# Kernel tuning notes

Hardware: AMD Instinct MI355X
Metric: run time of the kernel (lower is better)

## Reference

```python
import jax, jax.numpy as jnp
import numpy as np

B, L, D, H = 2, 2048, 2048, 16
Dh = D // H
THETA = 10000.0
NEG = -1e9


def _rope_tables(length, offset=0):
    # inv_freq: [Dh/2], positions: [L]
    inv_freq = 1.0 / (THETA ** (jnp.arange(0, Dh, 2, dtype=jnp.float32) / Dh))
    pos = jnp.arange(offset, offset + length, dtype=jnp.float32)
    freqs = pos[:, None] * inv_freq[None, :]           # [L, Dh/2]
    emb = jnp.concatenate([freqs, freqs], axis=-1)     # [L, Dh]
    return jnp.cos(emb), jnp.sin(emb)


def _rotate_half(t):
    t1, t2 = t[..., : Dh // 2], t[..., Dh // 2:]
    return jnp.concatenate([-t2, t1], axis=-1)


def setup_inputs() -> dict:
    key = jax.random.key(0)
    k1, k2, k3 = jax.random.split(key, 3)
    x = jax.random.normal(k1, (B, L, D), dtype=jnp.float32)
    attention_mask = jnp.ones((B, L), dtype=jnp.int32)
    w_qkv = jax.random.normal(k2, (D, 3 * D), dtype=jnp.float32) * (D ** -0.5)
    w_proj = jax.random.normal(k3, (D, D), dtype=jnp.float32) * (D ** -0.5)
    return {"x": x, "attention_mask": attention_mask, "w_qkv": w_qkv, "w_proj": w_proj}


def reference(x, attention_mask, w_qkv, w_proj):
    # QKV projection (no bias)
    qkv = x @ w_qkv                                    # [B, L, 3D]
    q, k, v = jnp.split(qkv, 3, axis=-1)
    q = q.reshape(B, L, H, Dh).transpose(0, 2, 1, 3)   # [B, H, L, Dh]
    k = k.reshape(B, L, H, Dh).transpose(0, 2, 1, 3)
    v = v.reshape(B, L, H, Dh).transpose(0, 2, 1, 3)

    # RoPE (past_len = 0)
    cos, sin = _rope_tables(L)                         # [L, Dh]
    q = q * cos + _rotate_half(q) * sin
    k = k * cos + _rotate_half(k) * sin

    # causal + key-padding mask (True = masked out)
    causal = jnp.triu(jnp.ones((L, L), dtype=bool), k=1)         # [L, L]
    pad = (attention_mask == 0)[:, None, None, :]                # [B,1,1,L]
    mask = causal[None, None, :, :] | pad                        # [B,1,L,L]

    scale = Dh ** -0.5
    scores = jnp.einsum("bhqd,bhkd->bhqk", q, k) * scale         # [B,H,L,L]
    scores = jnp.where(mask, NEG, scores)
    attn = jax.nn.softmax(scores, axis=-1)
    y = jnp.einsum("bhqk,bhkd->bhqd", attn, v)                   # [B,H,L,Dh]
    y = y.transpose(0, 2, 1, 3).reshape(B, L, D)
    return y @ w_proj
```

## Files before the change

kernel.cpp:

```cpp
#include <hip/hip_runtime.h>
#include <hip/hip_bf16.h>

typedef unsigned short ushort_t;
typedef __attribute__((ext_vector_type(4))) float fvec4;
typedef __attribute__((ext_vector_type(16))) float fvec16;
typedef __attribute__((ext_vector_type(8))) short short8;
typedef __attribute__((ext_vector_type(4))) unsigned short usvec4;
typedef __attribute__((ext_vector_type(2))) unsigned int uvec2;

typedef const __attribute__((address_space(1))) void* gas_ptr;
typedef __attribute__((address_space(3))) void* las_ptr;

__device__ __forceinline__ void glds16(const void* g, void* l) {
  __builtin_amdgcn_global_load_lds((gas_ptr)g, (las_ptr)l, 16, 0, 0);
}

__device__ __forceinline__ ushort_t f2bf(float f) {
  unsigned u = __float_as_uint(f);
  u += 0x7FFFu + ((u >> 16) & 1u);
  return (ushort_t)(u >> 16);
}
__device__ __forceinline__ float bf2f(ushort_t h) {
  return __uint_as_float(((unsigned)h) << 16);
}

__device__ __forceinline__ void swap32(unsigned& a, unsigned& b) {
#if __has_builtin(__builtin_amdgcn_permlane32_swap)
  uvec2 r = __builtin_amdgcn_permlane32_swap(a, b, false, false);
  a = r[0]; b = r[1];
#else
  const unsigned sa = (unsigned)__shfl_xor((int)a, 32);
  const unsigned sb = (unsigned)__shfl_xor((int)b, 32);
  const bool hi = (threadIdx.x & 32) != 0;
  const unsigned na = hi ? sb : a;
  const unsigned nb = hi ? b : sa;
  a = na; b = nb;
#endif
}

__global__ __launch_bounds__(256) void cast_f32_bf16(const float* __restrict__ X,
                                                     ushort_t* __restrict__ Xb) {
  const size_t i = ((size_t)blockIdx.x * 256 + threadIdx.x) * 4;
  const fvec4 v = *(const fvec4*)(X + i);
  usvec4 o;
  o[0] = f2bf(v[0]); o[1] = f2bf(v[1]); o[2] = f2bf(v[2]); o[3] = f2bf(v[3]);
  *(usvec4*)(Xb + i) = o;
}

__global__ __launch_bounds__(256) void tcast(const float* __restrict__ W,
                                             ushort_t* __restrict__ Wt,
                                             const int Kd, const int Nd) {
  __shared__ float ls[64][65];
  const int t = threadIdx.x;
  const int n0 = blockIdx.x * 64, k0 = blockIdx.y * 64;
  const int kr = t >> 4, nc = (t & 15) * 4;
#pragma unroll
  for (int it = 0; it < 4; ++it) {
    const fvec4 v = *(const fvec4*)(W + (size_t)(k0 + it * 16 + kr) * Nd + n0 + nc);
    ls[it * 16 + kr][nc + 0] = v[0];
    ls[it * 16 + kr][nc + 1] = v[1];
    ls[it * 16 + kr][nc + 2] = v[2];
    ls[it * 16 + kr][nc + 3] = v[3];
  }
  __syncthreads();
  const int nr = t >> 2, kg = (t & 3) * 16;
  __align__(16) ushort_t tmp[16];
#pragma unroll
  for (int i = 0; i < 16; ++i) tmp[i] = f2bf(ls[kg + i][nr]);
  ushort_t* dst = Wt + (size_t)(n0 + nr) * Kd + k0 + kg;
  *(short8*)(dst)     = *(const short8*)(tmp);
  *(short8*)(dst + 8) = *(const short8*)(tmp + 8);
}

#define FENCE asm volatile("" ::: "memory")

__device__ __forceinline__ void stage_unit(const ushort_t* __restrict__ G, const int rbase,
                                           const int K, const int tk,
                                           ushort_t* ldsmat, const int u,
                                           const int wv, const int lane) {
  const int rr = lane >> 3;
  const int kk = ((lane & 7) ^ rr) * 8;
  const int r64 = wv * 8 + rr;
  glds16(G + (size_t)(rbase + u * 64 + r64) * K + tk + kk,
         ldsmat + (((u * 2 + 0) * 64 + wv * 8) * 64));
  glds16(G + (size_t)(rbase + 128 + u * 64 + r64) * K + tk + kk,
         ldsmat + (((u * 2 + 1) * 64 + wv * 8) * 64));
}

__device__ __forceinline__ short8 frag_ld(const ushort_t* ldsmat, const int rbase,
                                          const int kc, const int quad, const int mm) {
  const int r = rbase + mm;
  const int blk = r >> 6;
  const int pblk = ((blk & 1) << 1) | (blk >> 1);
  const int ldsrow = pblk * 64 + (r & 63);
  const int kb = (kc * 64 + quad * 16) ^ ((mm & 7) << 4);
  return *(const short8*)(ldsmat + ldsrow * 64 + (kb >> 1));
}

#define LD_A4(s_, q_)                                                         \
  short8 af[2][2];                                                            \
  af[0][0] = frag_ld(&lds[s_][0][0], wr * 128 + (q_) * 32,      0, quad, mm); \
  af[0][1] = frag_ld(&lds[s_][0][0], wr * 128 + (q_) * 32,      1, quad, mm); \
  af[1][0] = frag_ld(&lds[s_][0][0], wr * 128 + (q_) * 32 + 16, 0, quad, mm); \
  af[1][1] = frag_ld(&lds[s_][0][0], wr * 128 + (q_) * 32 + 16, 1, quad, mm);

#define LD_B8(s_)                                                             \
  _Pragma("unroll")                                                           \
  for (int j = 0; j < 4; ++j) {                                               \
    bfr[j][0] = frag_ld(&lds[s_][1][0], wc * 64 + j * 16, 0, quad, mm);       \
    bfr[j][1] = frag_ld(&lds[s_][1][0], wc * 64 + j * 16, 1, quad, mm);       \
  }

#define MFMA16(q_)                                                            \
  __builtin_amdgcn_s_setprio(1);                                              \
  _Pragma("unroll")                                                           \
  for (int ii = 0; ii < 2; ++ii)                                              \
  _Pragma("unroll")                                                           \
  for (int j = 0; j < 4; ++j) {                                               \
    acc[(q_) * 2 + ii][j] = __builtin_amdgcn_mfma_f32_16x16x32_bf16(          \
        af[ii][0], bfr[j][0], acc[(q_) * 2 + ii][j], 0, 0, 0);                \
    acc[(q_) * 2 + ii][j] = __builtin_amdgcn_mfma_f32_16x16x32_bf16(          \
        af[ii][1], bfr[j][1], acc[(q_) * 2 + ii][j], 0, 0, 0);                \
  }                                                                           \
  __builtin_amdgcn_s_setprio(0);

__global__ __launch_bounds__(512, 2) void gemm256(
    const ushort_t* __restrict__ A, const ushort_t* __restrict__ Bt,
    const int M, const int N, const int K, const int mode,
    float* __restrict__ C,
    ushort_t* __restrict__ Qo, ushort_t* __restrict__ Ko, ushort_t* __restrict__ Vo) {
  __shared__ __align__(16) ushort_t lds[2][2][16384];

  const int tid = threadIdx.x, wv = tid >> 6, lane = tid & 63;
  const int quad = lane >> 4, mm = lane & 15;
  const int wr = wv >> 2, wc = wv & 3;

  const int nwg = gridDim.x, ntx = N >> 8;
  const int bid = blockIdx.x;
  const int swz = (bid & 7) * (nwg >> 3) + (bid >> 3);
  const int by = swz / ntx, bx = swz - by * ntx;
  const int row0 = by * 256, col0 = bx * 256;

  fvec4 acc[8][4];
#pragma unroll
  for (int i = 0; i < 8; ++i)
#pragma unroll
    for (int j = 0; j < 4; ++j) acc[i][j] = (fvec4){0.f, 0.f, 0.f, 0.f};

  short8 bfr[4][2];

  stage_unit(Bt, col0, K, 0,  &lds[0][1][0], 0, wv, lane); FENCE;
  stage_unit(Bt, col0, K, 0,  &lds[0][1][0], 1, wv, lane); FENCE;
  stage_unit(A,  row0, K, 0,  &lds[0][0][0], 0, wv, lane); FENCE;
  stage_unit(A,  row0, K, 0,  &lds[0][0][0], 1, wv, lane); FENCE;
  stage_unit(Bt, col0, K, 64, &lds[1][1][0], 0, wv, lane); FENCE;
  stage_unit(Bt, col0, K, 64, &lds[1][1][0], 1, wv, lane); FENCE;
  stage_unit(A,  row0, K, 64, &lds[1][0][0], 0, wv, lane); FENCE;
  asm volatile("s_waitcnt vmcnt(6)" ::: "memory");
  __builtin_amdgcn_s_barrier();

  const int nit = K >> 7;
  for (int i = 0; i < nit; ++i) {
    const bool more = (i + 1 < nit);
    const int kA = i * 128 + 64;
    const int kB = i * 128 + 128;
    const int kC = i * 128 + 192;
    { __builtin_amdgcn_s_barrier();
      LD_A4(0, 0); LD_B8(0);
      stage_unit(A, row0, K, kA, &lds[1][0][0], 1, wv, lane);
      MFMA16(0); }
    { __builtin_amdgcn_s_barrier();
      LD_A4(0, 1);
      if (more) stage_unit(Bt, col0, K, kB, &lds[0][1][0], 0, wv, lane);
      MFMA16(1); }
    { __builtin_amdgcn_s_barrier();
      LD_A4(0, 2);
      if (more) stage_unit(Bt, col0, K, kB, &lds[0][1][0], 1, wv, lane);
      MFMA16(2); }
    { __builtin_amdgcn_s_barrier();
      LD_A4(0, 3);
      if (more) { stage_unit(A, row0, K, kB, &lds[0][0][0], 0, wv, lane);
        asm volatile("s_waitcnt vmcnt(6)" ::: "memory");
      } else { asm volatile("s_waitcnt vmcnt(0)" ::: "memory"); }
      MFMA16(3); }
    { __builtin_amdgcn_s_barrier();
      LD_A4(1, 0); LD_B8(1);
      if (more) stage_unit(A, row0, K, kB, &lds[0][0][0], 1, wv, lane);
      MFMA16(0); }
    { __builtin_amdgcn_s_barrier();
      LD_A4(1, 1);
      if (more) stage_unit(Bt, col0, K, kC, &lds[1][1][0], 0, wv, lane);
      MFMA16(1); }
    { __builtin_amdgcn_s_barrier();
      LD_A4(1, 2);
      if (more) stage_unit(Bt, col0, K, kC, &lds[1][1][0], 1, wv, lane);
      MFMA16(2); }
    { __builtin_amdgcn_s_barrier();
      LD_A4(1, 3);
      if (more) { stage_unit(A, row0, K, kC, &lds[1][0][0], 0, wv, lane);
        asm volatile("s_waitcnt vmcnt(6)" ::: "memory"); }
      MFMA16(3); }
  }

  if (mode == 0) {
#pragma unroll
    for (int i = 0; i < 8; ++i)
#pragma unroll
      for (int r = 0; r < 4; ++r) {
        const int row = row0 + wr * 128 + i * 16 + quad * 4 + r;
        float* cr = C + (size_t)row * N + col0 + wc * 64;
#pragma unroll
        for (int j = 0; j < 4; ++j) cr[j * 16 + mm] = acc[i][j][r];
      }
  } else {
    const int gcol = col0 + wc * 64;
    const int which = gcol >> 11;
    const int h = (gcol >> 7) & 15;
    const int coff = gcol & 127;
    ushort_t* dst = (which == 0) ? Qo : (which == 1) ? Ko : Vo;
#pragma unroll
    for (int i = 0; i < 8; ++i)
#pragma unroll
      for (int r = 0; r < 4; ++r) {
        const int row = row0 + wr * 128 + i * 16 + quad * 4 + r;
        const int bb = row >> 11, l = row & 2047;
        ushort_t* dr = dst + ((size_t)(bb * 16 + h) * 2048 + l) * 128 + coff;
#pragma unroll
        for (int j = 0; j < 4; ++j) dr[j * 16 + mm] = f2bf(acc[i][j][r]);
      }
  }
}

__device__ __forceinline__ void stage_a128(const ushort_t* __restrict__ G, const int row0,
                                           const int K, const int tk, ushort_t* ldsA,
                                           const int wv, const int lane) {
  const int rr = lane >> 3;
  const int kk = ((lane & 7) ^ rr) * 8;
  const int r = wv * 8 + rr;
  glds16(G + (size_t)(row0 + r) * K + tk + kk,      ldsA + (wv * 8) * 64);
  glds16(G + (size_t)(row0 + 64 + r) * K + tk + kk, ldsA + (64 + wv * 8) * 64);
}
__device__ __forceinline__ void stage_b128(const ushort_t* __restrict__ G, const int col0,
                                           const int K, const int tk, ushort_t* ldsB,
                                           const int u, const int wv, const int lane) {
  const int rr = lane >> 3;
  const int kk = ((lane & 7) ^ rr) * 8;
  const int r = u * 64 + wv * 8 + rr;
  glds16(G + (size_t)(col0 + r) * K + tk + kk,       ldsB + (u * 64 + wv * 8) * 64);
  glds16(G + (size_t)(col0 + 128 + r) * K + tk + kk, ldsB + (128 + u * 64 + wv * 8) * 64);
}
__device__ __forceinline__ short8 fragld128(const ushort_t* mat, const int row,
                                            const int kc, const int quad) {
  const int kb = (kc * 64 + quad * 16) ^ ((row & 7) << 4);
  return *(const short8*)(mat + row * 64 + (kb >> 1));
}

__global__ __launch_bounds__(512, 2) void gemm128(
    const ushort_t* __restrict__ A, const ushort_t* __restrict__ Bt,
    const int M, const int N, const int K, const int mode,
    float* __restrict__ C,
    ushort_t* __restrict__ Qo, ushort_t* __restrict__ Ko, ushort_t* __restrict__ Vo) {
  __shared__ __align__(16) ushort_t l128[2][24576];

  const int tid = threadIdx.x, wv = tid >> 6, lane = tid & 63;
  const int quad = lane >> 4, mm = lane & 15;
  const int wr = wv >> 2, wc = wv & 3;

  const int nwg = gridDim.x, ntx = N >> 8;
  const int bid = blockIdx.x;
  const int swz = (bid & 7) * (nwg >> 3) + (bid >> 3);
  const int by = swz / ntx, bx = swz - by * ntx;
  const int row0 = by * 128, col0 = bx * 256;

  fvec4 acc[4][4];
#pragma unroll
  for (int m = 0; m < 4; ++m)
#pragma unroll
    for (int j = 0; j < 4; ++j) acc[m][j] = (fvec4){0.f, 0.f, 0.f, 0.f};

  ushort_t* A0 = &l128[0][0];     ushort_t* B0 = &l128[0][8192];
  ushort_t* A1 = &l128[1][0];     ushort_t* B1 = &l128[1][8192];

  short8 bfr[4][2];

  stage_b128(Bt, col0, K, 0,  B0, 0, wv, lane); FENCE;
  stage_b128(Bt, col0, K, 0,  B0, 1, wv, lane); FENCE;
  stage_a128(A,  row0, K, 0,  A0,    wv, lane); FENCE;
  stage_b128(Bt, col0, K, 64, B1, 0, wv, lane); FENCE;
  stage_b128(Bt, col0, K, 64, B1, 1, wv, lane); FENCE;
  asm volatile("s_waitcnt vmcnt(4)" ::: "memory");
  __builtin_amdgcn_s_barrier();

  const int nit = K >> 7;
  for (int i = 0; i < nit; ++i) {
    const bool more = (i + 1 < nit);
    const int kA = i * 128 + 64;
    const int kB = i * 128 + 128;
    const int kC = i * 128 + 192;
    {
      stage_a128(A, row0, K, kA, A1, wv, lane);
      short8 af[4];
#pragma unroll
      for (int m = 0; m < 4; ++m) af[m] = fragld128(A0, wr * 64 + m * 16 + mm, 0, quad);
#pragma unroll
      for (int j = 0; j < 4; ++j) {
        bfr[j][0] = fragld128(B0, wc * 64 + j * 16 + mm, 0, quad);
        bfr[j][1] = fragld128(B0, wc * 64 + j * 16 + mm, 1, quad);
      }
      __builtin_amdgcn_s_setprio(1);
#pragma unroll
      for (int m = 0; m < 4; ++m)
#pragma unroll
        for (int j = 0; j < 4; ++j)
          acc[m][j] = __builtin_amdgcn_mfma_f32_16x16x32_bf16(af[m], bfr[j][0], acc[m][j], 0, 0, 0);
      __builtin_amdgcn_s_setprio(0);
      asm volatile("s_waitcnt lgkmcnt(0)" ::: "memory");
      __builtin_amdgcn_sched_barrier(0);
    }
    {
      __builtin_amdgcn_s_barrier();
      if (more) { stage_b128(Bt, col0, K, kB, B0, 0, wv, lane); FENCE;
                  stage_b128(Bt, col0, K, kB, B0, 1, wv, lane); FENCE; }
      if (more) { asm volatile("s_waitcnt vmcnt(4)" ::: "memory"); }
      else      { asm volatile("s_waitcnt vmcnt(0)" ::: "memory"); }
      short8 af[4];
#pragma unroll
      for (int m = 0; m < 4; ++m) af[m] = fragld128(A0, wr * 64 + m * 16 + mm, 1, quad);
      __builtin_amdgcn_s_setprio(1);
#pragma unroll
      for (int m = 0; m < 4; ++m)
#pragma unroll
        for (int j = 0; j < 4; ++j)
          acc[m][j] = __builtin_amdgcn_mfma_f32_16x16x32_bf16(af[m], bfr[j][1], acc[m][j], 0, 0, 0);
      __builtin_amdgcn_s_setprio(0);
    }
    {
      __builtin_amdgcn_s_barrier();
      if (more) stage_a128(A, row0, K, kB, A0, wv, lane);
      short8 af[4];
#pragma unroll
      for (int m = 0; m < 4; ++m) af[m] = fragld128(A1, wr * 64 + m * 16 + mm, 0, quad);
#pragma unroll
      for (int j = 0; j < 4; ++j) {
        bfr[j][0] = fragld128(B1, wc * 64 + j * 16 + mm, 0, quad);
        bfr[j][1] = fragld128(B1, wc * 64 + j * 16 + mm, 1, quad);
      }
      __builtin_amdgcn_s_setprio(1);
#pragma unroll
      for (int m = 0; m < 4; ++m)
#pragma unroll
        for (int j = 0; j < 4; ++j)
          acc[m][j] = __builtin_amdgcn_mfma_f32_16x16x32_bf16(af[m], bfr[j][0], acc[m][j], 0, 0, 0);
      __builtin_amdgcn_s_setprio(0);
      asm volatile("s_waitcnt lgkmcnt(0)" ::: "memory");
      __builtin_amdgcn_sched_barrier(0);
    }
    {
      __builtin_amdgcn_s_barrier();
      if (more) { stage_b128(Bt, col0, K, kC, B1, 0, wv, lane); FENCE;
                  stage_b128(Bt, col0, K, kC, B1, 1, wv, lane); FENCE;
                  asm volatile("s_waitcnt vmcnt(4)" ::: "memory"); }
      short8 af[4];
#pragma unroll
      for (int m = 0; m < 4; ++m) af[m] = fragld128(A1, wr * 64 + m * 16 + mm, 1, quad);
      __builtin_amdgcn_s_setprio(1);
#pragma unroll
      for (int m = 0; m < 4; ++m)
#pragma unroll
        for (int j = 0; j < 4; ++j)
          acc[m][j] = __builtin_amdgcn_mfma_f32_16x16x32_bf16(af[m], bfr[j][1], acc[m][j], 0, 0, 0);
      __builtin_amdgcn_s_setprio(0);
      __builtin_amdgcn_s_barrier();
    }
  }

  if (mode == 0) {
#pragma unroll
    for (int m = 0; m < 4; ++m)
#pragma unroll
      for (int r = 0; r < 4; ++r) {
        const int row = row0 + wr * 64 + m * 16 + quad * 4 + r;
        float* cr = C + (size_t)row * N + col0 + wc * 64;
#pragma unroll
        for (int j = 0; j < 4; ++j) cr[j * 16 + mm] = acc[m][j][r];
      }
  } else {
    const int gcol = col0 + wc * 64;
    const int which = gcol >> 11;
    const int h = (gcol >> 7) & 15;
    const int coff = gcol & 127;
    ushort_t* dst = (which == 0) ? Qo : (which == 1) ? Ko : Vo;
#pragma unroll
    for (int m = 0; m < 4; ++m)
#pragma unroll
      for (int r = 0; r < 4; ++r) {
        const int row = row0 + wr * 64 + m * 16 + quad * 4 + r;
        const int bb = row >> 11, l = row & 2047;
        ushort_t* dr = dst + ((size_t)(bb * 16 + h) * 2048 + l) * 128 + coff;
#pragma unroll
        for (int j = 0; j < 4; ++j) dr[j * 16 + mm] = f2bf(acc[m][j][r]);
      }
  }
}

__global__ __launch_bounds__(256) void rope_kernel(ushort_t* Qb, ushort_t* Kb) {
  const int gid = blockIdx.x * 256 + threadIdx.x;
  const int pd = gid & 63;
  const int row = gid >> 6;
  const int l = row & 2047;
  ushort_t* base = (blockIdx.y ? Kb : Qb) + (size_t)row * 128;
  const float a = bf2f(base[pd]);
  const float bv = bf2f(base[pd + 64]);
  const float invf_rev = exp2f(-(float)pd * 0.20762050593045702f) * 0.15915494309189535f;
  float rev = (float)l * invf_rev;
  rev -= floorf(rev);
  const float ang = rev * 6.283185307179586f;
  float s, c;
  __sincosf(ang, &s, &c);
  float na = a * c - bv * s;
  float nb = bv * c + a * s;
  if (blockIdx.y == 0) { na *= 0.08838834764831845f; nb *= 0.08838834764831845f; }
  base[pd] = f2bf(na);
  base[pd + 64] = f2bf(nb);
}

__global__ __launch_bounds__(256) void vtrans_kernel(const ushort_t* __restrict__ Vn,
                                                     ushort_t* __restrict__ Vt) {
  __shared__ ushort_t ls[128 * 132];
  const int bh = blockIdx.x >> 4;
  const int l0 = (blockIdx.x & 15) * 128;
  const int t = threadIdx.x;
  const ushort_t* src = Vn + ((size_t)bh * 2048 + l0) * 128;
#pragma unroll
  for (int it = 0; it < 16; ++it) {
    const int c = it * 256 + t;
    const int lr = c >> 5, dc = (c & 31) * 4;
    *(usvec4*)(ls + lr * 132 + dc) = *(const usvec4*)(src + lr * 128 + dc);
  }
  __syncthreads();
  ushort_t* dstb = Vt + (size_t)bh * 128 * 2048 + l0;
#pragma unroll
  for (int it = 0; it < 16; ++it) {
    const int c = it * 256 + t;
    const int d = c >> 5, lc = (c & 31) * 4;
    usvec4 o;
    o[0] = ls[(lc + 0) * 132 + d];
    o[1] = ls[(lc + 1) * 132 + d];
    o[2] = ls[(lc + 2) * 132 + d];
    o[3] = ls[(lc + 3) * 132 + d];
    *(usvec4*)(dstb + (size_t)d * 2048 + lc) = o;
  }
}

__global__ __launch_bounds__(256, 2) void flash_kernel(
    const ushort_t* __restrict__ Qb, const ushort_t* __restrict__ Kb,
    const ushort_t* __restrict__ Vt, const int* __restrict__ am,
    ushort_t* __restrict__ Y) {
  __shared__ __align__(16) ushort_t lK[2][8192];
  __shared__ __align__(16) ushort_t lV[2][8192];
  __shared__ float lds_l[128];

  const int tid = threadIdx.x, wv = tid >> 6, lane = tid & 63;
  const int lh = lane >> 5, cq = lane & 31;
  const int bid = blockIdx.x;
  const int bh = bid & 31;
  const int qi = 15 - (bid >> 5);
  const int b = bh >> 4, head = bh & 15;
  const size_t qkBase = (size_t)bh * (2048 * 128);
  const int qb = qi * 128 + wv * 32;
  const int q = qb + cq;

  unsigned fullbits = 0;
  {
    const int* amr = am + b * 2048;
#pragma unroll
    for (int rgn = 0; rgn < 4; ++rgn) {
      const int4 a0 = *(const int4*)(amr + rgn * 512 + lane * 8);
      const int4 a1 = *(const int4*)(amr + rgn * 512 + lane * 8 + 4);
      const bool ok8 = a0.x && a0.y && a0.z && a0.w && a1.x && a1.y && a1.z && a1.w;
      const unsigned long long bal = __ballot(ok8);
#pragma unroll
      for (int tt = 0; tt < 8; ++tt)
        fullbits |= ((((bal >> (8 * tt)) & 0xFFull) == 0xFFull) ? 1u : 0u) << (rgn * 8 + tt);
    }
  }

  short8 qf[8];
  {
    const ushort_t* qrow = Qb + qkBase + (size_t)q * 128;
#pragma unroll
    for (int c = 0; c < 8; ++c) qf[c] = *(const short8*)(qrow + c * 16 + lh * 8);
  }

  fvec16 yacc[4];
#pragma unroll
  for (int i = 0; i < 4; ++i)
#pragma unroll
    for (int r = 0; r < 16; ++r) yacc[i][r] = 0.f;
  float psum = 0.f;

#define FLASH_STAGE(dK, dV, kk0)                                                          \
  _Pragma("unroll")                                                                       \
  for (int it = 0; it < 4; ++it) {                                                        \
    const int f_ = it * 4 + wv;                                                           \
    const int ct_ = f_ >> 3, c_ = f_ & 7;                                                 \
    glds16(Kb + qkBase + (size_t)((kk0) + ct_ * 32 + cq) * 128 + c_ * 16 + lh * 8,        \
           (dK) + f_ * 512);                                                              \
    const int dt_ = f_ >> 2, kc_ = f_ & 3;                                                \
    glds16(Vt + ((size_t)bh * 128 + dt_ * 32 + cq) * 2048 + (kk0) + kc_ * 16 + lh * 8,    \
           (dV) + f_ * 512);                                                              \
  }

  const int nt = qi * 2 + 2;
  FLASH_STAGE(&lK[0][0], &lV[0][0], 0)
  __syncthreads();

  int cur = 0;
  for (int t = 0; t < nt; ++t) {
    const int k0 = t * 64;
    if (t + 1 < nt) {
      FLASH_STAGE(&lK[cur ^ 1][0], &lV[cur ^ 1][0], k0 + 64)
    }

    if (k0 <= qb + 31) {
      const ushort_t* bK = &lK[cur][0];
      const ushort_t* bV = &lV[cur][0];
      const bool maskfull = (fullbits >> t) & 1u;
      unsigned long long keymask = ~0ull;
      if (!maskfull) keymask = __ballot(am[b * 2048 + k0 + lane] != 0);
      const bool fullvalid = (k0 + 63 <= qb) && maskfull;

#pragma unroll
      for (int ct = 0; ct < 2; ++ct) {
        fvec16 sA_, sB_;
#pragma unroll
        for (int r = 0; r < 16; ++r) { sA_[r] = 0.f; sB_[r] = 0.f; }
        __builtin_amdgcn_s_setprio(1);
#pragma unroll
        for (int c = 0; c < 4; ++c) {
          short8 kf = *(const short8*)(bK + (ct * 8 + c) * 512 + lane * 8);
          sA_ = __builtin_amdgcn_mfma_f32_32x32x16_bf16(kf, qf[c], sA_, 0, 0, 0);
        }
#pragma unroll
        for (int c = 4; c < 8; ++c) {
          short8 kf = *(const short8*)(bK + (ct * 8 + c) * 512 + lane * 8);
          sB_ = __builtin_amdgcn_mfma_f32_32x32x16_bf16(kf, qf[c], sB_, 0, 0, 0);
        }
        __builtin_amdgcn_s_setprio(0);
        float p[16];
        if (fullvalid) {
#pragma unroll
          for (int r = 0; r < 16; ++r) p[r] = __expf(sA_[r] + sB_[r]);
        } else {
#pragma unroll
          for (int r = 0; r < 16; ++r) {
            const int kl = (r & 3) + 8 * (r >> 2) + 4 * lh + ct * 32;
            const bool ok = (k0 + kl <= q) && (((keymask >> kl) & 1ull) != 0);
            p[r] = ok ? __expf(sA_[r] + sB_[r]) : 0.f;
          }
        }
#pragma unroll
        for (int r = 0; r < 16; ++r) psum += p[r];
        unsigned pk[8];
#pragma unroll
        for (int j = 0; j < 8; ++j) {
          __hip_bfloat162 t2 = __float22bfloat162_rn(make_float2(p[2 * j], p[2 * j + 1]));
          pk[j] = *(unsigned*)&t2;
        }
#pragma unroll
        for (int kc2 = 0; kc2 < 2; ++kc2) {
          unsigned a0 = pk[kc2 * 4 + 0], a2 = pk[kc2 * 4 + 2];
          unsigned a1 = pk[kc2 * 4 + 1], a3 = pk[kc2 * 4 + 3];
          swap32(a0, a2);
          swap32(a1, a3);
          union { unsigned u[4]; short8 s; } pf;
          pf.u[0] = a0; pf.u[1] = a1; pf.u[2] = a2; pf.u[3] = a3;
          const int kc = ct * 2 + kc2;
          __builtin_amdgcn_s_setprio(1);
#pragma unroll
          for (int dt = 0; dt < 4; ++dt) {
            short8 vf = *(const short8*)(bV + (dt * 4 + kc) * 512 + lane * 8);
            yacc[dt] = __builtin_amdgcn_mfma_f32_32x32x16_bf16(pf.s, vf, yacc[dt], 0, 0, 0);
          }
          __builtin_amdgcn_s_setprio(0);
        }
      }
    }
    __syncthreads();
    cur ^= 1;
  }
#undef FLASH_STAGE

  psum += __shfl_xor(psum, 32);
  if (lane < 32) lds_l[wv * 32 + lane] = psum;
  float inv16[16];
#pragma unroll
  for (int r = 0; r < 16; ++r)
    inv16[r] = 1.f / lds_l[wv * 32 + (r & 3) + 8 * (r >> 2) + 4 * lh];

#pragma unroll
  for (int dt = 0; dt < 4; ++dt)
#pragma unroll
    for (int r = 0; r < 16; ++r) {
      const int qloc = (r & 3) + 8 * (r >> 2) + 4 * lh;
      ushort_t* dst = Y + ((size_t)(b * 2048 + qb + qloc)) * 2048 + head * 128 + dt * 32 + cq;
      *dst = f2bf(yacc[dt][r] * inv16[r]);
    }
}

extern "C" void kernel_launch(void* const* d_in, const int* in_sizes, int n_in,
                              void* d_out, int out_size, void* d_ws, size_t ws_size,
                              hipStream_t stream) {
  const float* x      = (const float*)d_in[0];
  const int*   amask  = (const int*)d_in[1];
  const float* w_qkv  = (const float*)d_in[2];
  const float* w_proj = (const float*)d_in[3];

  ushort_t* xb     = (ushort_t*)d_ws;
  ushort_t* wqkvT  = xb + 8388608;
  ushort_t* wprojT = wqkvT + 12582912;
  ushort_t* Qb     = wprojT + 4194304;
  ushort_t* Kb     = Qb + 8388608;
  ushort_t* Vn     = Kb + 8388608;
  ushort_t* Vt     = wqkvT;
  ushort_t* Yb     = xb;

  cast_f32_bf16<<<8192, 256, 0, stream>>>(x, xb);
  tcast<<<dim3(96, 32), 256, 0, stream>>>(w_qkv, wqkvT, 2048, 6144);
  tcast<<<dim3(32, 32), 256, 0, stream>>>(w_proj, wprojT, 2048, 2048);
  gemm128<<<768, 512, 0, stream>>>(xb, wqkvT, 4096, 6144, 2048, 1,
                                   nullptr, Qb, Kb, Vn);
  rope_kernel<<<dim3(16384, 2), 256, 0, stream>>>(Qb, Kb);
  vtrans_kernel<<<512, 256, 0, stream>>>(Vn, Vt);
  flash_kernel<<<512, 256, 0, stream>>>(Qb, Kb, Vt, amask, Yb);
  gemm128<<<256, 512, 0, stream>>>(Yb, wprojT, 4096, 2048, 2048, 0,
                                   (float*)d_out, nullptr, nullptr, nullptr);
}
```

Measured before the change: 390.7 us.

## Replace 128x256 QKV GEMM with 256x192 tile kernel to balance CU waves

```diff
diff --git a/kernel.cpp b/kernel.cpp
--- a/kernel.cpp
+++ b/kernel.cpp
@@ -74,17 +74,13 @@
 
 #define FENCE asm volatile("" ::: "memory")
 
-__device__ __forceinline__ void stage_unit(const ushort_t* __restrict__ G, const int rbase,
-                                           const int K, const int tk,
-                                           ushort_t* ldsmat, const int u,
-                                           const int wv, const int lane) {
+__device__ __forceinline__ void stage_one(const ushort_t* __restrict__ G, const int grow,
+                                          const int K, const int tk, ushort_t* ldsmat,
+                                          const int lrow0, const int wv, const int lane) {
   const int rr = lane >> 3;
   const int kk = ((lane & 7) ^ rr) * 8;
-  const int r64 = wv * 8 + rr;
-  glds16(G + (size_t)(rbase + u * 64 + r64) * K + tk + kk,
-         ldsmat + (((u * 2 + 0) * 64 + wv * 8) * 64));
-  glds16(G + (size_t)(rbase + 128 + u * 64 + r64) * K + tk + kk,
-         ldsmat + (((u * 2 + 1) * 64 + wv * 8) * 64));
+  glds16(G + (size_t)(grow + wv * 8 + rr) * K + tk + kk,
+         ldsmat + (lrow0 + wv * 8) * 64);
 }
 
 __device__ __forceinline__ short8 frag_ld(const ushort_t* ldsmat, const int rbase,
@@ -97,26 +93,32 @@
   return *(const short8*)(ldsmat + ldsrow * 64 + (kb >> 1));
 }
 
-#define LD_A4(s_, q_)                                                         \
+__device__ __forceinline__ short8 fragld128(const ushort_t* mat, const int row,
+                                            const int kc, const int quad) {
+  const int kb = (kc * 64 + quad * 16) ^ ((row & 7) << 4);
+  return *(const short8*)(mat + row * 64 + (kb >> 1));
+}
+
+#define G192_LDA(Am, q_)                                                      \
   short8 af[2][2];                                                            \
-  af[0][0] = frag_ld(&lds[s_][0][0], wr * 128 + (q_) * 32,      0, quad, mm); \
-  af[0][1] = frag_ld(&lds[s_][0][0], wr * 128 + (q_) * 32,      1, quad, mm); \
-  af[1][0] = frag_ld(&lds[s_][0][0], wr * 128 + (q_) * 32 + 16, 0, quad, mm); \
-  af[1][1] = frag_ld(&lds[s_][0][0], wr * 128 + (q_) * 32 + 16, 1, quad, mm);
-
-#define LD_B8(s_)                                                             \
+  af[0][0] = frag_ld(Am, wr * 128 + (q_) * 32,      0, quad, mm);             \
+  af[0][1] = frag_ld(Am, wr * 128 + (q_) * 32,      1, quad, mm);             \
+  af[1][0] = frag_ld(Am, wr * 128 + (q_) * 32 + 16, 0, quad, mm);             \
+  af[1][1] = frag_ld(Am, wr * 128 + (q_) * 32 + 16, 1, quad, mm);
+
+#define G192_LDB(Bm)                                                          \
   _Pragma("unroll")                                                           \
-  for (int j = 0; j < 4; ++j) {                                               \
-    bfr[j][0] = frag_ld(&lds[s_][1][0], wc * 64 + j * 16, 0, quad, mm);       \
-    bfr[j][1] = frag_ld(&lds[s_][1][0], wc * 64 + j * 16, 1, quad, mm);       \
-  }
-
-#define MFMA16(q_)                                                            \
+  for (int j = 0; j < 3; ++j) {                                               \
+    bfr[j][0] = fragld128(Bm, wc * 48 + j * 16 + mm, 0, quad);                \
+    bfr[j][1] = fragld128(Bm, wc * 48 + j * 16 + mm, 1, quad);                \
+  }
+
+#define G192_MFMA(q_)                                                         \
   __builtin_amdgcn_s_setprio(1);                                              \
   _Pragma("unroll")                                                           \
   for (int ii = 0; ii < 2; ++ii)                                              \
   _Pragma("unroll")                                                           \
-  for (int j = 0; j < 4; ++j) {                                               \
+  for (int j = 0; j < 3; ++j) {                                               \
     acc[(q_) * 2 + ii][j] = __builtin_amdgcn_mfma_f32_16x16x32_bf16(          \
         af[ii][0], bfr[j][0], acc[(q_) * 2 + ii][j], 0, 0, 0);                \
     acc[(q_) * 2 + ii][j] = __builtin_amdgcn_mfma_f32_16x16x32_bf16(          \
@@ -124,39 +126,47 @@
   }                                                                           \
   __builtin_amdgcn_s_setprio(0);
 
-__global__ __launch_bounds__(512, 2) void gemm256(
+__global__ __launch_bounds__(512, 2) void gemm192(
     const ushort_t* __restrict__ A, const ushort_t* __restrict__ Bt,
     const int M, const int N, const int K, const int mode,
     float* __restrict__ C,
     ushort_t* __restrict__ Qo, ushort_t* __restrict__ Ko, ushort_t* __restrict__ Vo) {
-  __shared__ __align__(16) ushort_t lds[2][2][16384];
+  __shared__ __align__(16) ushort_t lds[2][28672];
 
   const int tid = threadIdx.x, wv = tid >> 6, lane = tid & 63;
   const int quad = lane >> 4, mm = lane & 15;
   const int wr = wv >> 2, wc = wv & 3;
 
-  const int nwg = gridDim.x, ntx = N >> 8;
+  const int nwg = gridDim.x, ntx = N / 192;
   const int bid = blockIdx.x;
   const int swz = (bid & 7) * (nwg >> 3) + (bid >> 3);
   const int by = swz / ntx, bx = swz - by * ntx;
-  const int row0 = by * 256, col0 = bx * 256;
-
-  fvec4 acc[8][4];
+  const int row0 = by * 256, col0 = bx * 192;
+
+  fvec4 acc[8][3];
 #pragma unroll
   for (int i = 0; i < 8; ++i)
 #pragma unroll
-    for (int j = 0; j < 4; ++j) acc[i][j] = (fvec4){0.f, 0.f, 0.f, 0.f};
-
-  short8 bfr[4][2];
-
-  stage_unit(Bt, col0, K, 0,  &lds[0][1][0], 0, wv, lane); FENCE;
-  stage_unit(Bt, col0, K, 0,  &lds[0][1][0], 1, wv, lane); FENCE;
-  stage_unit(A,  row0, K, 0,  &lds[0][0][0], 0, wv, lane); FENCE;
-  stage_unit(A,  row0, K, 0,  &lds[0][0][0], 1, wv, lane); FENCE;
-  stage_unit(Bt, col0, K, 64, &lds[1][1][0], 0, wv, lane); FENCE;
-  stage_unit(Bt, col0, K, 64, &lds[1][1][0], 1, wv, lane); FENCE;
-  stage_unit(A,  row0, K, 64, &lds[1][0][0], 0, wv, lane); FENCE;
-  asm volatile("s_waitcnt vmcnt(6)" ::: "memory");
+    for (int j = 0; j < 3; ++j) acc[i][j] = (fvec4){0.f, 0.f, 0.f, 0.f};
+
+  short8 bfr[3][2];
+
+  ushort_t* A0 = &lds[0][0];      ushort_t* B0 = &lds[0][16384];
+  ushort_t* A1 = &lds[1][0];      ushort_t* B1 = &lds[1][16384];
+
+  stage_one(Bt, col0 + 0,   K, 0,  B0, 0,   wv, lane); FENCE;
+  stage_one(Bt, col0 + 64,  K, 0,  B0, 64,  wv, lane); FENCE;
+  stage_one(Bt, col0 + 128, K, 0,  B0, 128, wv, lane); FENCE;
+  stage_one(A,  row0 + 0,   K, 0,  A0, 0,   wv, lane); FENCE;
+  stage_one(A,  row0 + 64,  K, 0,  A0, 128, wv, lane); FENCE;
+  stage_one(A,  row0 + 128, K, 0,  A0, 64,  wv, lane); FENCE;
+  stage_one(A,  row0 + 192, K, 0,  A0, 192, wv, lane); FENCE;
+  stage_one(Bt, col0 + 0,   K, 64, B1, 0,   wv, lane); FENCE;
+  stage_one(Bt, col0 + 64,  K, 64, B1, 64,  wv, lane); FENCE;
+  stage_one(Bt, col0 + 128, K, 64, B1, 128, wv, lane); FENCE;
+  stage_one(A,  row0 + 0,   K, 64, A1, 0,   wv, lane); FENCE;
+  stage_one(A,  row0 + 128, K, 64, A1, 64,  wv, lane); FENCE;
+  asm volatile("s_waitcnt vmcnt(5)" ::: "memory");
   __builtin_amdgcn_s_barrier();
 
   const int nit = K >> 7;
@@ -165,41 +175,70 @@
     const int kA = i * 128 + 64;
     const int kB = i * 128 + 128;
     const int kC = i * 128 + 192;
-    { __builtin_amdgcn_s_barrier();
-      LD_A4(0, 0); LD_B8(0);
-      stage_unit(A, row0, K, kA, &lds[1][0][0], 1, wv, lane);
-      MFMA16(0); }
-    { __builtin_amdgcn_s_barrier();
-      LD_A4(0, 1);
-      if (more) stage_unit(Bt, col0, K, kB, &lds[0][1][0], 0, wv, lane);
-      MFMA16(1); }
-    { __builtin_amdgcn_s_barrier();
-      LD_A4(0, 2);
-      if (more) stage_unit(Bt, col0, K, kB, &lds[0][1][0], 1, wv, lane);
-      MFMA16(2); }
-    { __builtin_amdgcn_s_barrier();
-      LD_A4(0, 3);
-      if (more) { stage_unit(A, row0, K, kB, &lds[0][0][0], 0, wv, lane);
-        asm volatile("s_waitcnt vmcnt(6)" ::: "memory");
-      } else { asm volatile("s_waitcnt vmcnt(0)" ::: "memory"); }
-      MFMA16(3); }
-    { __builtin_amdgcn_s_barrier();
-      LD_A4(1, 0); LD_B8(1);
-      if (more) stage_unit(A, row0, K, kB, &lds[0][0][0], 1, wv, lane);
-      MFMA16(0); }
-    { __builtin_amdgcn_s_barrier();
-      LD_A4(1, 1);
-      if (more) stage_unit(Bt, col0, K, kC, &lds[1][1][0], 0, wv, lane);
-      MFMA16(1); }
-    { __builtin_amdgcn_s_barrier();
-      LD_A4(1, 2);
-      if (more) stage_unit(Bt, col0, K, kC, &lds[1][1][0], 1, wv, lane);
-      MFMA16(2); }
-    { __builtin_amdgcn_s_barrier();
-      LD_A4(1, 3);
-      if (more) { stage_unit(A, row0, K, kC, &lds[1][0][0], 0, wv, lane);
-        asm volatile("s_waitcnt vmcnt(6)" ::: "memory"); }
-      MFMA16(3); }
+    {
+      __builtin_amdgcn_s_barrier();
+      G192_LDA(A0, 0);
+      G192_LDB(B0);
+      stage_one(A, row0 + 64,  K, kA, A1, 128, wv, lane); FENCE;
+      stage_one(A, row0 + 192, K, kA, A1, 192, wv, lane);
+      G192_MFMA(0);
+    }
+    {
+      __builtin_amdgcn_s_barrier();
+      G192_LDA(A0, 1);
+      if (more) { stage_one(Bt, col0 + 0,  K, kB, B0, 0,  wv, lane); FENCE;
+                  stage_one(Bt, col0 + 64, K, kB, B0, 64, wv, lane); }
+      G192_MFMA(1);
+    }
+    {
+      __builtin_amdgcn_s_barrier();
+      G192_LDA(A0, 2);
+      if (more) stage_one(Bt, col0 + 128, K, kB, B0, 128, wv, lane);
+      G192_MFMA(2);
+    }
+    {
+      __builtin_amdgcn_s_barrier();
+      G192_LDA(A0, 3);
+      if (more) {
+        stage_one(A, row0 + 0,   K, kB, A0, 0,  wv, lane); FENCE;
+        stage_one(A, row0 + 128, K, kB, A0, 64, wv, lane);
+        asm volatile("s_waitcnt vmcnt(5)" ::: "memory");
+      } else {
+        asm volatile("s_waitcnt vmcnt(0)" ::: "memory");
+      }
+      G192_MFMA(3);
+    }
+    {
+      __builtin_amdgcn_s_barrier();
+      G192_LDA(A1, 0);
+      G192_LDB(B1);
+      if (more) { stage_one(A, row0 + 64,  K, kB, A0, 128, wv, lane); FENCE;
+                  stage_one(A, row0 + 192, K, kB, A0, 192, wv, lane); }
+      G192_MFMA(0);
+    }
+    {
+      __builtin_amdgcn_s_barrier();
+      G192_LDA(A1, 1);
+      if (more) { stage_one(Bt, col0 + 0,  K, kC, B1, 0,  wv, lane); FENCE;
+                  stage_one(Bt, col0 + 64, K, kC, B1, 64, wv, lane); }
+      G192_MFMA(1);
+    }
+    {
+      __builtin_amdgcn_s_barrier();
+      G192_LDA(A1, 2);
+      if (more) stage_one(Bt, col0 + 128, K, kC, B1, 128, wv, lane);
+      G192_MFMA(2);
+    }
+    {
+      __builtin_amdgcn_s_barrier();
+      G192_LDA(A1, 3);
+      if (more) {
+        stage_one(A, row0 + 0,   K, kC, A1, 0,  wv, lane); FENCE;
+        stage_one(A, row0 + 128, K, kC, A1, 64, wv, lane);
+        asm volatile("s_waitcnt vmcnt(5)" ::: "memory");
+      }
+      G192_MFMA(3);
+    }
   }
 
   if (mode == 0) {
@@ -208,26 +247,27 @@
 #pragma unroll
       for (int r = 0; r < 4; ++r) {
         const int row = row0 + wr * 128 + i * 16 + quad * 4 + r;
-        float* cr = C + (size_t)row * N + col0 + wc * 64;
-#pragma unroll
-        for (int j = 0; j < 4; ++j) cr[j * 16 + mm] = acc[i][j][r];
+        float* cr = C + (size_t)row * N + col0 + wc * 48;
+#pragma unroll
+        for (int j = 0; j < 3; ++j) cr[j * 16 + mm] = acc[i][j][r];
       }
   } else {
-    const int gcol = col0 + wc * 64;
-    const int which = gcol >> 11;
-    const int h = (gcol >> 7) & 15;
-    const int coff = gcol & 127;
-    ushort_t* dst = (which == 0) ? Qo : (which == 1) ? Ko : Vo;
-#pragma unroll
-    for (int i = 0; i < 8; ++i)
-#pragma unroll
-      for (int r = 0; r < 4; ++r) {
-        const int row = row0 + wr * 128 + i * 16 + quad * 4 + r;
-        const int bb = row >> 11, l = row & 2047;
-        ushort_t* dr = dst + ((size_t)(bb * 16 + h) * 2048 + l) * 128 + coff;
-#pragma unroll
-        for (int j = 0; j < 4; ++j) dr[j * 16 + mm] = f2bf(acc[i][j][r]);
-      }
+#pragma unroll
+    for (int j = 0; j < 3; ++j) {
+      const int gcolj = col0 + wc * 48 + j * 16;
+      const int which = gcolj >> 11;
+      const int h = (gcolj >> 7) & 15;
+      const int coff = (gcolj & 127) + mm;
+      ushort_t* dst = (which == 0) ? Qo : (which == 1) ? Ko : Vo;
+#pragma unroll
+      for (int i = 0; i < 8; ++i)
+#pragma unroll
+        for (int r = 0; r < 4; ++r) {
+          const int row = row0 + wr * 128 + i * 16 + quad * 4 + r;
+          const int bb = row >> 11, l = row & 2047;
+          dst[((size_t)(bb * 16 + h) * 2048 + l) * 128 + coff] = f2bf(acc[i][j][r]);
+        }
+    }
   }
 }
 
@@ -248,11 +288,6 @@
   const int r = u * 64 + wv * 8 + rr;
   glds16(G + (size_t)(col0 + r) * K + tk + kk,       ldsB + (u * 64 + wv * 8) * 64);
   glds16(G + (size_t)(col0 + 128 + r) * K + tk + kk, ldsB + (128 + u * 64 + wv * 8) * 64);
-}
-__device__ __forceinline__ short8 fragld128(const ushort_t* mat, const int row,
-                                            const int kc, const int quad) {
-  const int kb = (kc * 64 + quad * 16) ^ ((row & 7) << 4);
-  return *(const short8*)(mat + row * 64 + (kb >> 1));
 }
 
 __global__ __launch_bounds__(512, 2) void gemm128(
@@ -628,7 +663,7 @@
   cast_f32_bf16<<<8192, 256, 0, stream>>>(x, xb);
   tcast<<<dim3(96, 32), 256, 0, stream>>>(w_qkv, wqkvT, 2048, 6144);
   tcast<<<dim3(32, 32), 256, 0, stream>>>(w_proj, wprojT, 2048, 2048);
-  gemm128<<<768, 512, 0, stream>>>(xb, wqkvT, 4096, 6144, 2048, 1,
+  gemm192<<<512, 512, 0, stream>>>(xb, wqkvT, 4096, 6144, 2048, 1,
                                    nullptr, Qb, Kb, Vn);
   rope_kernel<<<dim3(16384, 2), 256, 0, stream>>>(Qb, Kb);
   vtrans_kernel<<<512, 256, 0, stream>>>(Vn, Vt);
```

Result: no change. 383.1 us (-2.0%).
